# Optimization experiments

Hardware: AMD Instinct MI355X
Metric: run time of the kernel (lower is better)

## Reference

```python
import jax, jax.numpy as jnp
import numpy as np

D = 256          # object_dim == query_dim
HG = 1024        # g hidden / output width
HF0, HF1 = 1024, 512
OUT_F = 256
N = 32768        # number of objects


def _mlp_g(h, W0, b0, W1, b1, W2, b2):
    # g=True: ReLU after every layer, including output.
    h = jax.nn.relu(h @ W0 + b0)
    h = jax.nn.relu(h @ W1 + b1)
    return jax.nn.relu(h @ W2 + b2)


def _mlp_f(h, W0, b0, W1, b1, W2, b2):
    # f: ReLU on hidden layers, linear output.
    h = jax.nn.relu(h @ W0 + b0)
    h = jax.nn.relu(h @ W1 + b1)
    return h @ W2 + b2


def setup_inputs() -> dict:
    key = jax.random.key(0)
    ks = jax.random.split(key, 16)
    def lin(k, fan_in, fan_out):
        s = 1.0 / np.sqrt(fan_in)
        kw, kb = jax.random.split(k)
        W = jax.random.uniform(kw, (fan_in, fan_out), jnp.float32, -s, s)
        b = jax.random.uniform(kb, (fan_out,), jnp.float32, -s, s)
        return W, b
    x = jax.random.normal(ks[0], (N, D), jnp.float32)
    q = jax.random.normal(ks[1], (D,), jnp.float32)
    g_W0, g_b0 = lin(ks[2], 3 * D, HG)
    g_W1, g_b1 = lin(ks[3], HG, HG)
    g_W2, g_b2 = lin(ks[4], HG, HG)
    f_W0, f_b0 = lin(ks[5], HG, HF0)
    f_W1, f_b1 = lin(ks[6], HF0, HF1)
    f_W2, f_b2 = lin(ks[7], HF1, OUT_F)
    return dict(x=x, q=q,
                g_W0=g_W0, g_b0=g_b0, g_W1=g_W1, g_b1=g_b1, g_W2=g_W2, g_b2=g_b2,
                f_W0=f_W0, f_b0=f_b0, f_W1=f_W1, f_b1=f_b1, f_W2=f_W2, f_b2=f_b2)


def reference(x, q, g_W0, g_b0, g_W1, g_b1, g_W2, g_b2,
              f_W0, f_b0, f_W1, f_b1, f_W2, f_b2):
    n = x.shape[0]
    # mode 4: adjacent pairs (o_i, o_{i+1}), query concatenated to each pair.
    pair_concat = jnp.concatenate(
        [x[:-1], x[1:], jnp.broadcast_to(q, (n - 1, q.shape[0]))], axis=-1)  # (n-1, 3D)
    relations = _mlp_g(pair_concat, g_W0, g_b0, g_W1, g_b1, g_W2, g_b2)       # (n-1, HG)
    embedding = jnp.sum(relations, axis=0)                                     # (HG,)
    return _mlp_f(embedding, f_W0, f_b0, f_W1, f_b1, f_W2, f_b2)               # (OUT_F,)
```

## Files before the change

### kernel.cpp

```cpp
#include <hip/hip_runtime.h>

typedef __attribute__((ext_vector_type(8))) short short8;
typedef __attribute__((ext_vector_type(4))) float floatx4;
typedef __attribute__((ext_vector_type(4))) unsigned int uint32x4;

#define NROWS 32768L
#define NVALID 32767L
#define HGDIM 1024

__device__ __forceinline__ unsigned short f2bf_rne(float f) {
    union { float f; unsigned u; } v; v.f = f;
    unsigned r = v.u + 0x7fffu + ((v.u >> 16) & 1u);
    return (unsigned short)(r >> 16);
}

__device__ __forceinline__ void gload_lds16(const void* g, void* l) {
    __builtin_amdgcn_global_load_lds(
        (const __attribute__((address_space(1))) void*)g,
        (__attribute__((address_space(3))) void*)l,
        16, 0, 0);
}

__global__ void cvt_x(const float* __restrict__ x, unsigned short* __restrict__ xb,
                      long nx, long ntot4) {
    long i = (long)blockIdx.x * 256 + threadIdx.x;
    if (i >= ntot4) return;
    long i4 = i * 4;
    float4 v = make_float4(0.f, 0.f, 0.f, 0.f);
    if (i4 < nx) v = *(const float4*)(x + i4);
    ushort4 o;
    o.x = f2bf_rne(v.x); o.y = f2bf_rne(v.y); o.z = f2bf_rne(v.z); o.w = f2bf_rne(v.w);
    *(ushort4*)(xb + i4) = o;
}

__global__ void transpose_cvt(const float* __restrict__ W, unsigned short* __restrict__ Wt,
                              int K, int N) {
    __shared__ float tile[32][33];
    int tx = threadIdx.x & 31, ty = threadIdx.x >> 5;
    int nb = blockIdx.x * 32, kb = blockIdx.y * 32;
    #pragma unroll
    for (int i = 0; i < 32; i += 8)
        tile[ty + i][tx] = W[(size_t)(kb + ty + i) * N + (nb + tx)];
    __syncthreads();
    #pragma unroll
    for (int i = 0; i < 32; i += 8)
        Wt[(size_t)(nb + ty + i) * K + (kb + tx)] = f2bf_rne(tile[tx][ty + i]);
}

template<bool RELU_IN>
__global__ void fc_partial(const float* __restrict__ in, const float* __restrict__ W,
                           const float* __restrict__ bias, float* __restrict__ out,
                           int N) {
    __shared__ float s_in[128];
    int j = blockIdx.x * 256 + threadIdx.x;
    int k0 = blockIdx.y * 128;
    if (threadIdx.x < 128) {
        float v = in[k0 + threadIdx.x];
        if (RELU_IN) v = fmaxf(v, 0.f);
        s_in[threadIdx.x] = v;
    }
    __syncthreads();
    float acc = (blockIdx.y == 0) ? bias[j] : 0.f;
    #pragma unroll 4
    for (int k = 0; k < 128; ++k)
        acc += s_in[k] * W[(size_t)(k0 + k) * N + j];
    atomicAdd(&out[j], acc);
}


#define SBAR() __builtin_amdgcn_sched_barrier(0)

#define P_PRE(N) do { SBAR(); __builtin_amdgcn_s_barrier(); \
    asm volatile("s_waitcnt lgkmcnt(" #N ")" ::: "memory"); SBAR(); \
    __builtin_amdgcn_s_setprio(1); } while (0)

#define P_POST() do { __builtin_amdgcn_s_setprio(0); SBAR(); \
    __builtin_amdgcn_s_barrier(); } while (0)

#define P_POSTC(N) do { __builtin_amdgcn_s_setprio(0); SBAR(); \
    asm volatile("s_waitcnt vmcnt(" #N ")" ::: "memory"); SBAR(); \
    __builtin_amdgcn_s_barrier(); SBAR(); } while (0)

#define STAGE(buf, region, T) do { \
    if ((region) >= 2) { \
        const unsigned short* _g = gA + (long)(((region) & 1) * 128) * lda + (long)(T) * 64; \
        char* _d = (char*)&lds[buf][0][((region) & 1) * 128][0] + t * 16; \
        gload_lds16(_g, _d); \
        gload_lds16(_g + 64L * lda, _d + 8192); \
    } else { \
        const unsigned short* _g = gB + (long)(((region) & 1) * 128) * ldb + (long)(T) * 64; \
        char* _d = (char*)&lds[buf][1][((region) & 1) * 128][0] + t * 16; \
        gload_lds16(_g, _d); \
        gload_lds16(_g + 64L * ldb, _d + 8192); \
    } } while (0)

#define LDA4(dst, buf, mbase, ks) do { _Pragma("unroll") for (int _q = 0; _q < 4; ++_q) \
    dst[_q] = *(const short8*)((const char*)&lds[buf][0][arowb + ((mbase) + _q) * 16][0] + ((ks) ? cb1 : cb0)); } while (0)

#define LDB4(dst, buf, ks) do { _Pragma("unroll") for (int _q = 0; _q < 4; ++_q) \
    dst[_q] = *(const short8*)((const char*)&lds[buf][1][browb + _q * 16][0] + ((ks) ? cb1 : cb0)); } while (0)

#define MFMA16(AF, BF, MO) do { _Pragma("unroll") for (int _mf = 0; _mf < 4; ++_mf) { \
    _Pragma("unroll") for (int _nf = 0; _nf < 4; ++_nf) \
        acc[(MO) + _mf][_nf] = __builtin_amdgcn_mfma_f32_16x16x32_bf16(AF[_mf], BF[_nf], acc[(MO) + _mf][_nf], 0, 0, 0); } } while (0)

template<int COLSUM>
__global__ __launch_bounds__(512, 2)
void gemm256(const unsigned short* __restrict__ A, int lda,
             const unsigned short* __restrict__ Bt, int ldb,
             const float* __restrict__ bias, int K,
             unsigned short* __restrict__ Hout,
             float* __restrict__ emb, long row0g, long nvalid,
             int mblocks) {
    __shared__ alignas(16) unsigned short lds[2][2][256][64];

    const int t = threadIdx.x;
    int nwg = gridDim.x, bid = blockIdx.x, swz;
    if ((nwg & 7) == 0) { int cpx = nwg >> 3; swz = (bid & 7) * cpx + (bid >> 3); }
    else swz = bid;
    const int mb = swz >> 2, nb = swz & 3;
    const long m0 = (long)mb * 256;
    const int n0 = nb * 256;

    const int srow = t >> 3;
    const int ssc = (t & 7) ^ (srow & 7);
    const unsigned short* gA = A + (m0 + srow) * (long)lda + ssc * 8;
    const unsigned short* gB = Bt + ((long)n0 + srow) * (long)ldb + ssc * 8;

    const int lane = t & 63;
    const int wv = t >> 6;
    const int wm = wv >> 2, wn = wv & 3;
    const int arowb = wm * 128 + (lane & 15);
    const int browb = wn * 64 + (lane & 15);
    const int c0x = (lane >> 4) ^ (lane & 7);
    const int cb0 = c0x * 16;
    const int cb1 = (c0x ^ 4) * 16;

    floatx4 acc[8][4] = {};

    const int NT = K >> 6;
    const int NI = NT >> 1;

    short8 bE0[4], bE1[4], bO0[4], bO1[4];
    short8 aE0[4], aE1[4], aE2[4], aE3[4], aO0[4], aO1[4], aO2[4], aO3[4];

    STAGE(0, 0, 0); STAGE(0, 1, 0); STAGE(0, 2, 0); STAGE(0, 3, 0);
    STAGE(1, 0, 1); STAGE(1, 1, 1);
    asm volatile("s_waitcnt vmcnt(4)" ::: "memory");
    SBAR();
    __builtin_amdgcn_s_barrier();
    SBAR();
    LDB4(bE0, 0, 0); LDA4(aE0, 0, 0, 0);

    for (int i = 0; i < NI; ++i) {
        const int O = 2 * i + 1;
        int N2 = 2 * i + 2; if (N2 >= NT) N2 = 0;
        int P2 = 2 * i + 3; if (P2 >= NT) P2 = 1;

        LDA4(aE1, 0, 4, 0);
        P_PRE(4);
        STAGE(1, 2, O);
        MFMA16(aE0, bE0, 0);
        P_POST();
        LDB4(bE1, 0, 1); LDA4(aE2, 0, 0, 1);
        P_PRE(8);
        STAGE(1, 3, O);
        MFMA16(aE1, bE0, 4);
        P_POST();
        LDA4(aE3, 0, 4, 1);
        P_PRE(4);
        STAGE(0, 0, N2);
        MFMA16(aE2, bE1, 0);
        P_POSTC(2);
        LDB4(bO0, 1, 0); LDA4(aO0, 1, 0, 0);
        P_PRE(8);
        STAGE(0, 1, N2);
        MFMA16(aE3, bE1, 4);
        P_POST();
        LDA4(aO1, 1, 4, 0);
        P_PRE(4);
        STAGE(0, 2, N2);
        MFMA16(aO0, bO0, 0);
        P_POST();
        LDB4(bO1, 1, 1); LDA4(aO2, 1, 0, 1);
        P_PRE(8);
        STAGE(0, 3, N2);
        MFMA16(aO1, bO0, 4);
        P_POST();
        LDA4(aO3, 1, 4, 1);
        P_PRE(4);
        STAGE(1, 0, P2);
        MFMA16(aO2, bO1, 0);
        P_POSTC(2);
        LDB4(bE0, 0, 0); LDA4(aE0, 0, 0, 0);
        P_PRE(8);
        STAGE(1, 1, P2);
        MFMA16(aO3, bO1, 4);
        P_POST();
    }
    asm volatile("s_waitcnt vmcnt(0) lgkmcnt(0)" ::: "memory");
    SBAR();
    __builtin_amdgcn_s_barrier();

    if (COLSUM == 0) {
        char* slb = (char*)&lds[0][0][0][0];
        #pragma unroll
        for (int nf = 0; nf < 4; ++nf) {
            int ncol = wn * 64 + nf * 16 + (lane & 15);
            float bv = bias[n0 + ncol];
            #pragma unroll
            for (int mf = 0; mf < 8; ++mf) {
                int rbase = wm * 128 + mf * 16 + ((lane >> 4) << 2);
                #pragma unroll
                for (int j = 0; j < 4; ++j) {
                    int row = rbase + j;
                    float v = fmaxf(acc[mf][nf][j] + bv, 0.f);
                    int byte = row * 512 + ((ncol * 2) ^ ((row & 7) << 4));
                    *(unsigned short*)(slb + byte) = f2bf_rne(v);
                }
            }
        }
        __syncthreads();
        {
            int rsub = t >> 5;
            int cb = (t & 31) * 16;
            #pragma unroll
            for (int i2 = 0; i2 < 16; ++i2) {
                int row = i2 * 16 + rsub;
                const char* src = slb + row * 512 + (cb ^ ((row & 7) << 4));
                uint32x4 v = *(const uint32x4*)src;
                char* dst = (char*)Hout + ((size_t)(m0 + row) * HGDIM + n0) * 2 + cb;
                *(uint32x4*)dst = v;
            }
        }
    } else {
        #pragma unroll
        for (int nf = 0; nf < 4; ++nf) {
            int ncol = n0 + wn * 64 + nf * 16 + (lane & 15);
            float bv = bias[ncol];
            float cs = 0.f;
            #pragma unroll
            for (int mf = 0; mf < 8; ++mf) {
                long rbase = row0g + m0 + wm * 128 + mf * 16 + ((lane >> 4) << 2);
                #pragma unroll
                for (int j = 0; j < 4; ++j) {
                    float v = fmaxf(acc[mf][nf][j] + bv, 0.f);
                    if (rbase + j < nvalid) cs += v;
                }
            }
            cs += __shfl_xor(cs, 16);
            cs += __shfl_xor(cs, 32);
            if ((lane >> 4) == 0) atomicAdd(&emb[ncol], cs);
        }
    }
}

extern "C" void kernel_launch(void* const* d_in, const int* in_sizes, int n_in,
                              void* d_out, int out_size, void* d_ws, size_t ws_size,
                              hipStream_t stream) {
    const float* x   = (const float*)d_in[0];
    const float* q   = (const float*)d_in[1];
    const float* gW0 = (const float*)d_in[2];
    const float* gb0 = (const float*)d_in[3];
    const float* gW1 = (const float*)d_in[4];
    const float* gb1 = (const float*)d_in[5];
    const float* gW2 = (const float*)d_in[6];
    const float* gb2 = (const float*)d_in[7];
    const float* fW0 = (const float*)d_in[8];
    const float* fb0 = (const float*)d_in[9];
    const float* fW1 = (const float*)d_in[10];
    const float* fb1 = (const float*)d_in[11];
    const float* fW2 = (const float*)d_in[12];
    const float* fb2 = (const float*)d_in[13];
    float* out = (float*)d_out;

    char* ws = (char*)d_ws;
    size_t off = 0;
    auto alloc = [&](size_t bytes) -> char* {
        char* p = ws + off;
        off += (bytes + 255) & ~(size_t)255;
        return p;
    };
    unsigned short* xb  = (unsigned short*)alloc((NROWS + 1) * 256 * 2);
    unsigned short* w0t = (unsigned short*)alloc((size_t)1024 * 512 * 2);
    unsigned short* w1t = (unsigned short*)alloc((size_t)1024 * 1024 * 2);
    unsigned short* w2t = (unsigned short*)alloc((size_t)1024 * 1024 * 2);
    float* c0  = (float*)alloc(4096);
    float* emb = (float*)alloc(4096);
    float* e1  = (float*)alloc(4096);
    float* e2  = (float*)alloc(4096);
    size_t fixed = off;
    size_t avail = (ws_size > fixed) ? ws_size - fixed : 0;
    long CR = (long)((avail / 2) / (HGDIM * 2));
    CR = (CR / 512) * 512;
    if (CR > NROWS) CR = NROWS;
    if (CR < 512) CR = 512;
    unsigned short* H0 = (unsigned short*)alloc((size_t)CR * HGDIM * 2);
    unsigned short* H1 = (unsigned short*)alloc((size_t)CR * HGDIM * 2);

    hipMemsetAsync(c0, 0, 4 * 4096, stream);
    hipMemsetAsync(out, 0, 256 * sizeof(float), stream);

    long ntot4 = (NROWS + 1) * 256 / 4;
    cvt_x<<<dim3((unsigned)((ntot4 + 255) / 256)), 256, 0, stream>>>(x, xb, NROWS * 256, ntot4);

    transpose_cvt<<<dim3(32, 16), 256, 0, stream>>>(gW0, w0t, 512, 1024);
    transpose_cvt<<<dim3(32, 32), 256, 0, stream>>>(gW1, w1t, 1024, 1024);
    transpose_cvt<<<dim3(32, 32), 256, 0, stream>>>(gW2, w2t, 1024, 1024);

    fc_partial<false><<<dim3(4, 2), 256, 0, stream>>>(q, gW0 + (size_t)512 * 1024, gb0, c0, 1024);

    for (long r0 = 0; r0 < NROWS; r0 += CR) {
        long rows = NROWS - r0; if (rows > CR) rows = CR;
        int mblocks = (int)(rows / 256);
        dim3 g((unsigned)(mblocks * 4));
        gemm256<0><<<g, 512, 0, stream>>>(xb + r0 * 256, 256, w0t, 512, c0, 512,
                                          H0, nullptr, 0, 0, mblocks);
        gemm256<0><<<g, 512, 0, stream>>>(H0, 1024, w1t, 1024, gb1, 1024,
                                          H1, nullptr, 0, 0, mblocks);
        gemm256<1><<<g, 512, 0, stream>>>(H1, 1024, w2t, 1024, gb2, 1024,
                                          nullptr, emb, r0, NVALID, mblocks);
    }

    fc_partial<false><<<dim3(4, 8), 256, 0, stream>>>(emb, fW0, fb0, e1, 1024);
    fc_partial<true><<<dim3(2, 8), 256, 0, stream>>>(e1, fW1, fb1, e2, 512);
    fc_partial<true><<<dim3(1, 4), 256, 0, stream>>>(e2, fW2, fb2, out, 256);
}
```

Measured before the change: 243.2 us.

## Fuse prep kernels into one launch and simplify GEMM phase synchronization

Merges the x conversion, three weight transpose-converts and the query bias partial product into a single prep kernel that dispatches on block index, so fewer launches are needed. In the GEMM main loop, the fine-grained lgkmcnt/vmcnt waits are replaced by a uniform pattern: full LDS wait plus barrier before each phase, and a vmcnt(2) wait plus barrier after it. This makes the schedule simpler but more conservative, because LDS reads no longer overlap with the MFMA phase that follows them. It also adds vmcnt waits after every phase.

```diff
diff --git a/kernel.cpp b/kernel.cpp
--- a/kernel.cpp
+++ b/kernel.cpp
@@ -21,30 +21,62 @@
         16, 0, 0);
 }
 
-__global__ void cvt_x(const float* __restrict__ x, unsigned short* __restrict__ xb,
-                      long nx, long ntot4) {
-    long i = (long)blockIdx.x * 256 + threadIdx.x;
-    if (i >= ntot4) return;
-    long i4 = i * 4;
-    float4 v = make_float4(0.f, 0.f, 0.f, 0.f);
-    if (i4 < nx) v = *(const float4*)(x + i4);
-    ushort4 o;
-    o.x = f2bf_rne(v.x); o.y = f2bf_rne(v.y); o.z = f2bf_rne(v.z); o.w = f2bf_rne(v.w);
-    *(ushort4*)(xb + i4) = o;
-}
-
-__global__ void transpose_cvt(const float* __restrict__ W, unsigned short* __restrict__ Wt,
-                              int K, int N) {
-    __shared__ float tile[32][33];
-    int tx = threadIdx.x & 31, ty = threadIdx.x >> 5;
-    int nb = blockIdx.x * 32, kb = blockIdx.y * 32;
+#define NB_CVT 8193
+#define NB_T0  512
+#define NB_T1  1024
+#define NB_T2  1024
+
+__global__ void prep(const float* __restrict__ x, unsigned short* __restrict__ xb,
+                     const float* __restrict__ gW0, unsigned short* __restrict__ w0t,
+                     const float* __restrict__ gW1, unsigned short* __restrict__ w1t,
+                     const float* __restrict__ gW2, unsigned short* __restrict__ w2t,
+                     const float* __restrict__ q, const float* __restrict__ gb0,
+                     float* __restrict__ c0) {
+    __shared__ float smem[1056];
+    int b = blockIdx.x, tid = threadIdx.x;
+    if (b < NB_CVT) {
+        long i = (long)b * 256 + tid;
+        long ntot4 = (NROWS + 1) * 64;
+        if (i < ntot4) {
+            long i4 = i * 4, nx = NROWS * 256;
+            float4 v = make_float4(0.f, 0.f, 0.f, 0.f);
+            if (i4 < nx) v = *(const float4*)(x + i4);
+            ushort4 o;
+            o.x = f2bf_rne(v.x); o.y = f2bf_rne(v.y);
+            o.z = f2bf_rne(v.z); o.w = f2bf_rne(v.w);
+            *(ushort4*)(xb + i4) = o;
+        }
+        return;
+    }
+    b -= NB_CVT;
+    const float* W; unsigned short* Wt; int K, N;
+    if (b < NB_T0)                  { W = gW0; Wt = w0t; K = 512;  N = 1024; }
+    else if (b < NB_T0 + NB_T1)     { b -= NB_T0; W = gW1; Wt = w1t; K = 1024; N = 1024; }
+    else if (b < NB_T0 + NB_T1 + NB_T2) { b -= NB_T0 + NB_T1; W = gW2; Wt = w2t; K = 1024; N = 1024; }
+    else {
+        b -= NB_T0 + NB_T1 + NB_T2;
+        int bx = b & 3, by = b >> 2;
+        int j = bx * 256 + tid, k0 = by * 128;
+        if (tid < 128) smem[tid] = q[k0 + tid];
+        __syncthreads();
+        float a = (by == 0) ? gb0[j] : 0.f;
+        #pragma unroll 4
+        for (int k = 0; k < 128; ++k)
+            a += smem[k] * gW0[(size_t)(512 + k0 + k) * 1024 + j];
+        atomicAdd(&c0[j], a);
+        return;
+    }
+    int bx = b & 31, by = b >> 5;
+    float (*tile)[33] = (float(*)[33])smem;
+    int tx = tid & 31, ty = tid >> 5;
+    int nb2 = bx * 32, kb = by * 32;
     #pragma unroll
     for (int i = 0; i < 32; i += 8)
-        tile[ty + i][tx] = W[(size_t)(kb + ty + i) * N + (nb + tx)];
+        tile[ty + i][tx] = W[(size_t)(kb + ty + i) * N + (nb2 + tx)];
     __syncthreads();
     #pragma unroll
     for (int i = 0; i < 32; i += 8)
-        Wt[(size_t)(nb + ty + i) * K + (kb + tx)] = f2bf_rne(tile[tx][ty + i]);
+        Wt[(size_t)(nb2 + ty + i) * K + (kb + tx)] = f2bf_rne(tile[tx][ty + i]);
 }
 
 template<bool RELU_IN>
@@ -70,16 +102,13 @@
 
 #define SBAR() __builtin_amdgcn_sched_barrier(0)
 
-#define P_PRE(N) do { SBAR(); __builtin_amdgcn_s_barrier(); \
-    asm volatile("s_waitcnt lgkmcnt(" #N ")" ::: "memory"); SBAR(); \
+#define S_PRE() do { SBAR(); __builtin_amdgcn_s_barrier(); \
+    asm volatile("s_waitcnt lgkmcnt(0)" ::: "memory"); SBAR(); \
     __builtin_amdgcn_s_setprio(1); } while (0)
 
-#define P_POST() do { __builtin_amdgcn_s_setprio(0); SBAR(); \
+#define S_POST() do { __builtin_amdgcn_s_setprio(0); SBAR(); \
+    asm volatile("s_waitcnt vmcnt(2)" ::: "memory"); \
     __builtin_amdgcn_s_barrier(); } while (0)
-
-#define P_POSTC(N) do { __builtin_amdgcn_s_setprio(0); SBAR(); \
-    asm volatile("s_waitcnt vmcnt(" #N ")" ::: "memory"); SBAR(); \
-    __builtin_amdgcn_s_barrier(); SBAR(); } while (0)
 
 #define STAGE(buf, region, T) do { \
     if ((region) >= 2) { \
@@ -106,12 +135,12 @@
 
 template<int COLSUM>
 __global__ __launch_bounds__(512, 2)
-void gemm256(const unsigned short* __restrict__ A, int lda,
-             const unsigned short* __restrict__ Bt, int ldb,
-             const float* __restrict__ bias, int K,
-             unsigned short* __restrict__ Hout,
-             float* __restrict__ emb, long row0g, long nvalid,
-             int mblocks) {
+void gemmS(const unsigned short* __restrict__ A, int lda,
+           const unsigned short* __restrict__ Bt, int ldb,
+           const float* __restrict__ bias, int K,
+           unsigned short* __restrict__ Hout,
+           float* __restrict__ emb, long row0g, long nvalid,
+           int mblocks) {
     __shared__ alignas(16) unsigned short lds[2][2][256][64];
 
     const int t = threadIdx.x;
@@ -157,46 +186,46 @@
         int N2 = 2 * i + 2; if (N2 >= NT) N2 = 0;
         int P2 = 2 * i + 3; if (P2 >= NT) P2 = 1;
 
+        S_PRE();
         LDA4(aE1, 0, 4, 0);
-        P_PRE(4);
         STAGE(1, 2, O);
         MFMA16(aE0, bE0, 0);
-        P_POST();
+        S_POST();
+        S_PRE();
         LDB4(bE1, 0, 1); LDA4(aE2, 0, 0, 1);
-        P_PRE(8);
         STAGE(1, 3, O);
         MFMA16(aE1, bE0, 4);
-        P_POST();
+        S_POST();
+        S_PRE();
         LDA4(aE3, 0, 4, 1);
-        P_PRE(4);
         STAGE(0, 0, N2);
         MFMA16(aE2, bE1, 0);
-        P_POSTC(2);
+        S_POST();
+        S_PRE();
         LDB4(bO0, 1, 0); LDA4(aO0, 1, 0, 0);
-        P_PRE(8);
         STAGE(0, 1, N2);
         MFMA16(aE3, bE1, 4);
-        P_POST();
+        S_POST();
+        S_PRE();
         LDA4(aO1, 1, 4, 0);
-        P_PRE(4);
         STAGE(0, 2, N2);
         MFMA16(aO0, bO0, 0);
-        P_POST();
+        S_POST();
+        S_PRE();
         LDB4(bO1, 1, 1); LDA4(aO2, 1, 0, 1);
-        P_PRE(8);
         STAGE(0, 3, N2);
         MFMA16(aO1, bO0, 4);
-        P_POST();
+        S_POST();
+        S_PRE();
         LDA4(aO3, 1, 4, 1);
-        P_PRE(4);
         STAGE(1, 0, P2);
         MFMA16(aO2, bO1, 0);
-        P_POSTC(2);
+        S_POST();
+        S_PRE();
         LDB4(bE0, 0, 0); LDA4(aE0, 0, 0, 0);
-        P_PRE(8);
         STAGE(1, 1, P2);
         MFMA16(aO3, bO1, 4);
-        P_POST();
+        S_POST();
     }
     asm volatile("s_waitcnt vmcnt(0) lgkmcnt(0)" ::: "memory");
     SBAR();
@@ -301,25 +330,19 @@
     hipMemsetAsync(c0, 0, 4 * 4096, stream);
     hipMemsetAsync(out, 0, 256 * sizeof(float), stream);
 
-    long ntot4 = (NROWS + 1) * 256 / 4;
-    cvt_x<<<dim3((unsigned)((ntot4 + 255) / 256)), 256, 0, stream>>>(x, xb, NROWS * 256, ntot4);
-
-    transpose_cvt<<<dim3(32, 16), 256, 0, stream>>>(gW0, w0t, 512, 1024);
-    transpose_cvt<<<dim3(32, 32), 256, 0, stream>>>(gW1, w1t, 1024, 1024);
-    transpose_cvt<<<dim3(32, 32), 256, 0, stream>>>(gW2, w2t, 1024, 1024);
-
-    fc_partial<false><<<dim3(4, 2), 256, 0, stream>>>(q, gW0 + (size_t)512 * 1024, gb0, c0, 1024);
+    prep<<<dim3(NB_CVT + NB_T0 + NB_T1 + NB_T2 + 8), 256, 0, stream>>>(
+        x, xb, gW0, w0t, gW1, w1t, gW2, w2t, q, gb0, c0);
 
     for (long r0 = 0; r0 < NROWS; r0 += CR) {
         long rows = NROWS - r0; if (rows > CR) rows = CR;
         int mblocks = (int)(rows / 256);
         dim3 g((unsigned)(mblocks * 4));
-        gemm256<0><<<g, 512, 0, stream>>>(xb + r0 * 256, 256, w0t, 512, c0, 512,
-                                          H0, nullptr, 0, 0, mblocks);
-        gemm256<0><<<g, 512, 0, stream>>>(H0, 1024, w1t, 1024, gb1, 1024,
-                                          H1, nullptr, 0, 0, mblocks);
-        gemm256<1><<<g, 512, 0, stream>>>(H1, 1024, w2t, 1024, gb2, 1024,
-                                          nullptr, emb, r0, NVALID, mblocks);
+        gemmS<0><<<g, 512, 0, stream>>>(xb + r0 * 256, 256, w0t, 512, c0, 512,
+                                        H0, nullptr, 0, 0, mblocks);
+        gemmS<0><<<g, 512, 0, stream>>>(H0, 1024, w1t, 1024, gb1, 1024,
+                                        H1, nullptr, 0, 0, mblocks);
+        gemmS<1><<<g, 512, 0, stream>>>(H1, 1024, w2t, 1024, gb2, 1024,
+                                        nullptr, emb, r0, NVALID, mblocks);
     }
 
     fc_partial<false><<<dim3(4, 8), 256, 0, stream>>>(emb, fW0, fb0, e1, 1024);
```

Result: faster. 231.0 us (-5.0%).
